# Kernel tuning notes

Measured on AMD Instinct MI355X. Metric: run time of the kernel, lower is better.

The kernel has to match this reference:

```python
import jax, jax.numpy as jnp
from jax import lax
import numpy as np

ACTBIT = 8
B, CIN, COUT, H, W, K = 32, 16, 16, 256, 256, 3


def setup_inputs() -> dict:
    key = jax.random.key(0)
    k1, k2, k3, k4 = jax.random.split(key, 4)
    x = jax.random.normal(k1, (B, CIN, H, W), dtype=jnp.float32)
    # quantized int8 weight values stored as float (already deadzone-quantized + descaled ints)
    weight_int8 = jnp.round(jnp.clip(jax.random.normal(k2, (COUT, CIN, K, K)) * 40.0, -127.0, 127.0)).astype(jnp.float32)
    # per-output-channel power-of-two weight scale: 2**delta, delta in [-8, -4)
    delta = jax.random.randint(k3, (COUT,), -8, -4).astype(jnp.float32)
    scale_weight = jnp.exp2(delta).astype(jnp.float32)
    bias = jax.random.normal(k4, (COUT,), dtype=jnp.float32)
    return {"x": x, "weight_int8": weight_int8, "scale_weight": scale_weight, "bias": bias}


def reference(x, weight_int8, scale_weight, bias):
    n = 2.0 ** (ACTBIT - 1) - 1.0  # 127
    # channel-last, as in tochannellast
    x_cl = jnp.transpose(x, (0, 2, 3, 1))  # [B,H,W,Cin]
    # dynamic activation scale: max|x| / 2^(actbit-1)
    scale_input = jnp.max(jnp.abs(x_cl)) / (2.0 ** (ACTBIT - 1))
    # fast_qfn: div, clamp to [-n, n], round  (integer-valued activations)
    x_q = jnp.round(jnp.clip(x_cl / scale_input, -n, n))
    # int conv (emulated in fp32 on integer-valued tensors), stride 1, pad 1
    w_hwio = jnp.transpose(weight_int8, (2, 3, 1, 0))  # [K,K,Cin,Cout]
    acc = lax.conv_general_dilated(
        x_q, w_hwio, window_strides=(1, 1), padding=((1, 1), (1, 1)),
        dimension_numbers=("NHWC", "HWIO", "NHWC"))  # [B,H,W,Cout]
    # dequant: scalar input scale * per-output-channel weight scale, then bias
    out = acc * (scale_input * scale_weight) + bias
    # back to channel-first
    return jnp.transpose(out, (0, 3, 1, 2))
```

## Files before the change

kernel.cpp:

```cpp
#include <hip/hip_runtime.h>
#include <hip/hip_bf16.h>

#define B_    32
#define H_    256
#define W_    256
#define ROWS  8
#define LR    (ROWS + 2)
#define LCP   68
#define RSTR  (LCP*2)
#define BUFU  (LR*RSTR)
#define NT    8
#define NTILES (B_*(H_/ROWS)*(W_/64))
#define RAWB  (128*64)
#define RAWH  256

typedef float f32x4 __attribute__((ext_vector_type(4)));
typedef short s16x8 __attribute__((ext_vector_type(8)));
typedef unsigned int u32;

__device__ inline unsigned short f2bf(float f){
  __hip_bfloat16 h = __float2bfloat16(f);
  return __builtin_bit_cast(unsigned short, h);
}

__device__ inline float quant1(float v, float rinv, float s, float hs){
  float q0 = rintf(v * rinv);
  float d  = fmaf(q0, -s, v);
  q0 += (d >  hs) ? 1.f : 0.f;
  q0 -= (d < -hs) ? 1.f : 0.f;
  return fminf(fmaxf(q0, -127.f), 127.f);
}

__device__ __forceinline__ void tile_decode(int t, int& b, int& w0, int& h0){
  int hg = t & 31; int r = t >> 5;
  w0 = (r & 3) * 64; b = r >> 2; h0 = hg * ROWS;
}

__device__ __forceinline__ void build_packA(const float* __restrict__ wq,
                                            unsigned short* __restrict__ packA,
                                            int l){
  int co = l & 15;
  int g  = l >> 4;
  for (int mm2 = 0; mm2 < 5; ++mm2){
    for (int i = 0; i < 8; ++i){
      int kappa = g*8 + i;
      int tap = 2*mm2 + (kappa >> 4);
      int ci  = kappa & 15;
      float v = (tap <= 8) ? wq[(co*16 + ci)*9 + tap] : 0.f;
      packA[(mm2*64 + l)*8 + i] = f2bf(v);
    }
  }
}

__global__ __launch_bounds__(256) void absmax_kernel(const float* __restrict__ x,
                                                     const float* __restrict__ wq,
                                                     float* __restrict__ pmax,
                                                     unsigned short* __restrict__ packA,
                                                     int n4){
  __shared__ float red[4];
  int idx = blockIdx.x*blockDim.x + threadIdx.x;
  int stride = gridDim.x*blockDim.x;
  float m = 0.f;
  for (int i = idx; i < n4; i += stride){
    float4 v = reinterpret_cast<const float4*>(x)[i];
    m = fmaxf(m, fmaxf(fmaxf(fabsf(v.x), fabsf(v.y)), fmaxf(fabsf(v.z), fabsf(v.w))));
  }
  #pragma unroll
  for (int off = 32; off > 0; off >>= 1)
    m = fmaxf(m, __shfl_xor(m, off));
  int lane = threadIdx.x & 63, wid = threadIdx.x >> 6;
  if (lane == 0) red[wid] = m;
  __syncthreads();
  if (threadIdx.x == 0)
    pmax[blockIdx.x] = fmaxf(fmaxf(red[0], red[1]), fmaxf(red[2], red[3]));
  if (blockIdx.x == 0 && threadIdx.x < 64) build_packA(wq, packA, threadIdx.x);
}

__device__ __forceinline__ void q_load_full(const float* __restrict__ x,
                                            int b, int w0, int h0,
                                            int tid, int lane, int wid,
                                            float v[3][8], float tv[8]){
  const int c = lane;
  const int win = w0 - 1 + c;
  const bool colok = (unsigned)win < 256u;
  #pragma unroll
  for (int k = 0; k < 3; ++k){
    int gi = wid + 8*k;
    bool act = gi < 20;
    int r = gi >> 1, half = gi & 1;
    int hin = h0 + r - 1;
    bool rowok = (unsigned)hin < 256u;
    bool ok = act && rowok && colok;
    const float* p = x + ((size_t)(b*16 + half*8) << 16) + (size_t)(rowok ? hin : 0)*256 + win;
    #pragma unroll
    for (int ci = 0; ci < 8; ++ci)
      v[k][ci] = ok ? p[(size_t)ci << 16] : 0.f;
  }
  if (tid >= 448 && tid < 488){
    int t = tid - 448;
    int t_c = 64 + (t & 1), t_half = (t >> 1) & 1, t_r = t >> 2;
    int hin = h0 + t_r - 1;
    bool rowok = (unsigned)hin < 256u;
    int twin = w0 - 1 + t_c;
    bool ok = rowok && ((unsigned)twin < 256u);
    const float* p = x + ((size_t)(b*16 + t_half*8) << 16) + (size_t)(rowok ? hin : 0)*256 + twin;
    #pragma unroll
    for (int ci = 0; ci < 8; ++ci)
      tv[ci] = ok ? p[(size_t)ci << 16] : 0.f;
  }
}

__device__ __forceinline__ void q_write_full(s16x8* ldsv,
                                             int tid, int lane, int wid,
                                             const float v[3][8], const float tv[8],
                                             float rinv, float s, float hs){
  const int c = lane;
  #pragma unroll
  for (int k = 0; k < 3; ++k){
    int gi = wid + 8*k;
    if (gi < 20){
      int r = gi >> 1, half = gi & 1;
      s16x8 qv;
      #pragma unroll
      for (int ci = 0; ci < 8; ++ci)
        qv[ci] = (short)f2bf(quant1(v[k][ci], rinv, s, hs));
      int u = (r*RSTR + c*2 + half) ^ ((c >> 2) & 7);
      ldsv[u] = qv;
    }
  }
  if (tid >= 448 && tid < 488){
    int t = tid - 448;
    int t_c = 64 + (t & 1), t_half = (t >> 1) & 1, t_r = t >> 2;
    s16x8 qv;
    #pragma unroll
    for (int ci = 0; ci < 8; ++ci)
      qv[ci] = (short)f2bf(quant1(tv[ci], rinv, s, hs));
    int u = (t_r*RSTR + t_c*2 + t_half) ^ ((t_c >> 2) & 7);
    ldsv[u] = qv;
  }
}

__device__ __forceinline__ void dma_stage(const float* __restrict__ x,
                                          int b, int w0, int h02,
                                          int lane, int wid, u32* raw){
  int hin2 = h02 + wid + 1;
  int hinc = hin2 > 255 ? 255 : hin2;
  #pragma unroll
  for (int ci = 0; ci < 16; ++ci){
    const float* g = x + ((size_t)(b*16 + ci) << 16) + (size_t)hinc*256 + (w0 + lane);
    __builtin_amdgcn_global_load_lds(
        (const __attribute__((address_space(1))) u32*)g,
        (__attribute__((address_space(3))) u32*)(raw + (wid*16 + ci)*64), 4, 0, 0);
  }
  if (wid < 4){
    int e = wid*64 + lane;
    int p = e >> 1, side = e & 1;
    int rr = p >> 4, ci = p & 15;
    int hh = h02 + rr + 1; hh = hh > 255 ? 255 : hh;
    int win2 = side ? (w0 + 64) : (w0 - 1);
    win2 = win2 < 0 ? 0 : (win2 > 255 ? 255 : win2);
    const float* g = x + ((size_t)(b*16 + ci) << 16) + (size_t)hh*256 + win2;
    __builtin_amdgcn_global_load_lds(
        (const __attribute__((address_space(1))) u32*)g,
        (__attribute__((address_space(3))) u32*)(raw + RAWB + wid*64), 4, 0, 0);
  }
}

__device__ __forceinline__ void quant_pair(s16x8* ldsq, int bufoff, const u32* raw,
                                           int rr, int c, int half, bool rowok, int w0,
                                           float rinv, float s, float hs){
  bool ok = rowok && (c == 0 ? (w0 > 0) : (c == 65 ? (w0 < 192) : true));
  s16x8 qv;
  #pragma unroll
  for (int i = 0; i < 8; ++i){
    int ci = half*8 + i;
    int p  = rr*16 + ci;
    u32 bits = (c >= 1 && c <= 64) ? raw[p*64 + (c - 1)]
                                   : raw[RAWB + p*2 + (c != 0)];
    float val = ok ? __uint_as_float(bits) : 0.f;
    qv[i] = (short)f2bf(quant1(val, rinv, s, hs));
  }
  int r = rr + 2;
  int u = (r*RSTR + c*2 + half) ^ ((c >> 2) & 7);
  ldsq[bufoff + u] = qv;
}

__device__ __forceinline__ void quant_from_raw(s16x8* ldsq, int bufoff, const u32* raw,
                                               int lane, int wid, int w0, int h02,
                                               float rinv, float s, float hs){
  const int rr = wid;
  const bool rowok = (h02 + rr + 1) < 256;
  quant_pair(ldsq, bufoff, raw, rr, lane, 0, rowok, w0, rinv, s, hs);
  quant_pair(ldsq, bufoff, raw, rr, lane, 1, rowok, w0, rinv, s, hs);
  if (lane < 4)
    quant_pair(ldsq, bufoff, raw, rr, 64 + (lane >> 1), lane & 1, rowok, w0, rinv, s, hs);
}

__device__ __forceinline__ void c_phase(const s16x8* ldsv, int bufoff,
                                        const s16x8 A[5], const int kr[5], const int kw[5],
                                        int lane, int wid, int b, int w0, int h0,
                                        const float sc[4], const float bb[4],
                                        float* __restrict__ out){
  const int colg = lane & 15;
  const int g    = lane >> 4;
  const int hlf  = g & 1;
  f32x4 acc[4] = {};
  #pragma unroll
  for (int n = 0; n < 4; ++n){
    #pragma unroll
    for (int m = 0; m < 5; ++m){
      int cc = n*16 + colg + kw[m];
      int u = ((wid + kr[m])*RSTR + cc*2 + hlf) ^ ((cc >> 2) & 7);
      acc[n] = __builtin_amdgcn_mfma_f32_16x16x32_bf16(A[m], ldsv[bufoff + u], acc[n], 0, 0, 0);
    }
  }
  const int h = h0 + wid;
  #pragma unroll
  for (int j = 0; j < 4; ++j){
    const int co = g*4 + j;
    float* op = out + ((size_t)(b*16 + co) << 16) + h*256 + w0 + colg;
    #pragma unroll
    for (int n = 0; n < 4; ++n)
      __builtin_nontemporal_store(acc[n][j] * sc[j] + bb[j], op + n*16);
  }
}

__global__ __launch_bounds__(512)
void fconv_kernel(const float* __restrict__ x,
                  const float* __restrict__ sw,
                  const float* __restrict__ bias,
                  const float* __restrict__ pmax,
                  const unsigned short* __restrict__ packA,
                  float* __restrict__ out){
  __shared__ __align__(16) unsigned short lds_q[2*LR*LCP*16];
  __shared__ __align__(16) u32 lds_raw[RAWB + RAWH];
  __shared__ float redmax[8];
  s16x8* ldsq = reinterpret_cast<s16x8*>(lds_q);

  const int tid  = threadIdx.x;
  const int lane = tid & 63;
  const int wid  = tid >> 6;

  const int bid = blockIdx.x;
  const int t0  = (bid & 7)*512 + (bid >> 3)*NT;

  int b, w0, h0;
  float v[3][8], tv[8];

  tile_decode(t0, b, w0, h0);
  q_load_full(x, b, w0, h0, tid, lane, wid, v, tv);

  float4 pv = reinterpret_cast<const float4*>(pmax)[tid];
  float m = fmaxf(fmaxf(pv.x, pv.y), fmaxf(pv.z, pv.w));
  #pragma unroll
  for (int off = 32; off > 0; off >>= 1)
    m = fmaxf(m, __shfl_xor(m, off));
  if (lane == 0) redmax[wid] = m;
  __syncthreads();
  float gm = redmax[0];
  #pragma unroll
  for (int i = 1; i < 8; ++i) gm = fmaxf(gm, redmax[i]);

  const float s    = gm * 0.0078125f;
  const float rinv = 1.0f / s;
  const float hs   = 0.5f * s;

  const int g   = lane >> 4;
  const int tlg = g >> 1;
  int kr[5], kw[5];
  #pragma unroll
  for (int mm = 0; mm < 5; ++mm){
    int t = 2*mm + tlg; if (t > 8) t = 8;
    kr[mm] = (t*11) >> 5;
    kw[mm] = t - kr[mm]*3;
  }
  s16x8 A[5];
  const s16x8* pA = reinterpret_cast<const s16x8*>(packA);
  #pragma unroll
  for (int mm = 0; mm < 5; ++mm) A[mm] = pA[mm*64 + lane];
  float sc[4], bb[4];
  #pragma unroll
  for (int j = 0; j < 4; ++j){
    sc[j] = s * sw[g*4 + j];
    bb[j] = bias[g*4 + j];
  }

  q_write_full(ldsq, tid, lane, wid, v, tv, rinv, s, hs);
  __syncthreads();

  for (int k = 0; k < NT; ++k){
    const int cur = k & 1;
    if (k < NT-1){
      int b2, w2, h2; tile_decode(t0 + k + 1, b2, w2, h2);
      dma_stage(x, b2, w2, h2, lane, wid, lds_raw);
    }
    tile_decode(t0 + k, b, w0, h0);
    c_phase(ldsq, cur*BUFU, A, kr, kw, lane, wid, b, w0, h0, sc, bb, out);
    if (k < NT-1){
      __syncthreads();
      if (tid < 2*RSTR){
        int rr2 = tid >= RSTR;
        int cc2 = tid - rr2*RSTR;
        ldsq[(cur^1)*BUFU + rr2*RSTR + cc2] = ldsq[cur*BUFU + (8+rr2)*RSTR + cc2];
      }
      int b2, w2, h2; tile_decode(t0 + k + 1, b2, w2, h2);
      quant_from_raw(ldsq, (cur^1)*BUFU, lds_raw, lane, wid, w2, h2, rinv, s, hs);
      __syncthreads();
    }
  }
}

extern "C" void kernel_launch(void* const* d_in, const int* in_sizes, int n_in,
                              void* d_out, int out_size, void* d_ws, size_t ws_size,
                              hipStream_t stream){
  const float* x    = (const float*)d_in[0];
  const float* wq   = (const float*)d_in[1];
  const float* sw   = (const float*)d_in[2];
  const float* bias = (const float*)d_in[3];
  float* out = (float*)d_out;
  unsigned short* packA = (unsigned short*)((char*)d_ws + 64);
  float* pmax = (float*)((char*)d_ws + 8192);

  absmax_kernel<<<2048, 256, 0, stream>>>(x, wq, pmax, packA, (B_*16*H_*W_)/4);
  fconv_kernel<<<NTILES/NT, 512, 0, stream>>>(x, sw, bias, pmax, packA, out);
}
```

Baseline: 82.65 us.

## Use 16-byte LDS DMA loads and prefetch next raw tile earlier

Replaces the 4-byte per-channel global_load_lds with 16-byte wide loads, cutting the number of DMA instructions. The next-next tile's DMA is now issued right after the raw tile has been read into registers, so the global fetch overlaps the quantization and the following compute phase. Full syncthreads are replaced with hand-placed s_barrier and waitcnt calls, including vmcnt(16) to let outstanding stores drain partially. The raw LDS layout changes with the wide loads, while the reader still indexes it as lane-1 per channel, so correctness depends on the two layouts matching. The hand-tuned waitcnt counts are also a risk.

```diff
diff --git a/kernel.cpp b/kernel.cpp
--- a/kernel.cpp
+++ b/kernel.cpp
@@ -140,17 +140,20 @@
   }
 }
 
-__device__ __forceinline__ void dma_stage(const float* __restrict__ x,
-                                          int b, int w0, int h02,
-                                          int lane, int wid, u32* raw){
+__device__ __forceinline__ void dma_stage16(const float* __restrict__ x,
+                                            int b, int w0, int h02,
+                                            int lane, int wid, u32* raw){
   int hin2 = h02 + wid + 1;
   int hinc = hin2 > 255 ? 255 : hin2;
-  #pragma unroll
-  for (int ci = 0; ci < 16; ++ci){
-    const float* g = x + ((size_t)(b*16 + ci) << 16) + (size_t)hinc*256 + (w0 + lane);
+  int sub  = lane >> 4;
+  int c4   = (lane & 15) * 4;
+  #pragma unroll
+  for (int i = 0; i < 4; ++i){
+    int ci = i*4 + sub;
+    const float* g = x + ((size_t)(b*16 + ci) << 16) + (size_t)hinc*256 + (w0 + c4);
     __builtin_amdgcn_global_load_lds(
         (const __attribute__((address_space(1))) u32*)g,
-        (__attribute__((address_space(3))) u32*)(raw + (wid*16 + ci)*64), 4, 0, 0);
+        (__attribute__((address_space(3))) u32*)(raw + (wid*16 + i*4)*64), 16, 0, 0);
   }
   if (wid < 4){
     int e = wid*64 + lane;
@@ -185,15 +188,23 @@
   ldsq[bufoff + u] = qv;
 }
 
-__device__ __forceinline__ void quant_from_raw(s16x8* ldsq, int bufoff, const u32* raw,
-                                               int lane, int wid, int w0, int h02,
-                                               float rinv, float s, float hs){
-  const int rr = wid;
-  const bool rowok = (h02 + rr + 1) < 256;
-  quant_pair(ldsq, bufoff, raw, rr, lane, 0, rowok, w0, rinv, s, hs);
-  quant_pair(ldsq, bufoff, raw, rr, lane, 1, rowok, w0, rinv, s, hs);
-  if (lane < 4)
-    quant_pair(ldsq, bufoff, raw, rr, 64 + (lane >> 1), lane & 1, rowok, w0, rinv, s, hs);
+__device__ __forceinline__ void quant_main_regs(s16x8* ldsq, int bufoff,
+                                                const u32 r[16], int lane, int wid,
+                                                int w2, int h2,
+                                                float rinv, float s, float hs){
+  const bool rowok = (h2 + wid + 1) < 256;
+  const bool ok = rowok && (lane > 0 ? true : (w2 > 0));
+  #pragma unroll
+  for (int half = 0; half < 2; ++half){
+    s16x8 qv;
+    #pragma unroll
+    for (int i = 0; i < 8; ++i){
+      float val = ok ? __uint_as_float(r[half*8 + i]) : 0.f;
+      qv[i] = (short)f2bf(quant1(val, rinv, s, hs));
+    }
+    int u = ((wid + 2)*RSTR + lane*2 + half) ^ ((lane >> 2) & 7);
+    ldsq[bufoff + u] = qv;
+  }
 }
 
 __device__ __forceinline__ void c_phase(const s16x8* ldsv, int bufoff,
@@ -288,24 +299,56 @@
   q_write_full(ldsq, tid, lane, wid, v, tv, rinv, s, hs);
   __syncthreads();
 
+  {
+    int b2, w2, h2; tile_decode(t0 + 1, b2, w2, h2);
+    dma_stage16(x, b2, w2, h2, lane, wid, lds_raw);
+  }
+
   for (int k = 0; k < NT; ++k){
     const int cur = k & 1;
-    if (k < NT-1){
-      int b2, w2, h2; tile_decode(t0 + k + 1, b2, w2, h2);
-      dma_stage(x, b2, w2, h2, lane, wid, lds_raw);
-    }
     tile_decode(t0 + k, b, w0, h0);
     c_phase(ldsq, cur*BUFU, A, kr, kw, lane, wid, b, w0, h0, sc, bb, out);
     if (k < NT-1){
-      __syncthreads();
+      int b2, w2, h2; tile_decode(t0 + k + 1, b2, w2, h2);
+      const int nxt = (cur^1)*BUFU;
+      __builtin_amdgcn_sched_barrier(0);
+      asm volatile("s_waitcnt vmcnt(16)" ::: "memory");
+      asm volatile("s_waitcnt lgkmcnt(0)" ::: "memory");
+      __builtin_amdgcn_s_barrier();
+      __builtin_amdgcn_sched_barrier(0);
+
+      const bool rowok = (h2 + wid + 1) < 256;
+      u32 r[16];
+      #pragma unroll
+      for (int ci = 0; ci < 16; ++ci){
+        int p = wid*16 + ci;
+        r[ci] = (lane > 0) ? lds_raw[p*64 + (lane - 1)] : lds_raw[RAWB + p*2];
+      }
+      if (lane < 4)
+        quant_pair(ldsq, nxt, lds_raw, wid, 64 + (lane >> 1), lane & 1, rowok, w2, rinv, s, hs);
+
+      __builtin_amdgcn_sched_barrier(0);
+      asm volatile("s_waitcnt lgkmcnt(0)" ::: "memory");
+      __builtin_amdgcn_s_barrier();
+      __builtin_amdgcn_sched_barrier(0);
+
+      if (k < NT-2){
+        int b3, w3, h3; tile_decode(t0 + k + 2, b3, w3, h3);
+        dma_stage16(x, b3, w3, h3, lane, wid, lds_raw);
+      }
+      __builtin_amdgcn_sched_barrier(0);
+
       if (tid < 2*RSTR){
         int rr2 = tid >= RSTR;
         int cc2 = tid - rr2*RSTR;
-        ldsq[(cur^1)*BUFU + rr2*RSTR + cc2] = ldsq[cur*BUFU + (8+rr2)*RSTR + cc2];
+        ldsq[nxt + rr2*RSTR + cc2] = ldsq[cur*BUFU + (8+rr2)*RSTR + cc2];
       }
-      int b2, w2, h2; tile_decode(t0 + k + 1, b2, w2, h2);
-      quant_from_raw(ldsq, (cur^1)*BUFU, lds_raw, lane, wid, w2, h2, rinv, s, hs);
-      __syncthreads();
+      quant_main_regs(ldsq, nxt, r, lane, wid, w2, h2, rinv, s, hs);
+
+      __builtin_amdgcn_sched_barrier(0);
+      asm volatile("s_waitcnt lgkmcnt(0)" ::: "memory");
+      __builtin_amdgcn_s_barrier();
+      __builtin_amdgcn_sched_barrier(0);
     }
   }
 }
```

After: 77.70 us, median of 2. 1.06x faster.
